# Optimization experiments

Hardware: AMD Instinct MI355X
Metric: run time of the kernel (lower is better)

## Reference

```python
import jax, jax.numpy as jnp
import numpy as np


def _gcn_conv(x, edge_index, W, b):
    # PyG GCNConv: h = x @ W; out = D^{-1/2}(A+I)D^{-1/2} h + b
    N = x.shape[0]
    src, dst = edge_index[0], edge_index[1]
    # degree with self-loops (edge weights = 1)
    deg = jax.ops.segment_sum(jnp.ones(src.shape[0], x.dtype), dst, num_segments=N) + 1.0
    dis = jax.lax.rsqrt(deg)  # deg >= 1 so finite
    h = x @ W  # [N, F_out]
    norm = dis[src] * dis[dst]  # [E]
    msg = h[src] * norm[:, None]  # [E, F_out] -- dominant memory traffic
    agg = jax.ops.segment_sum(msg, dst, num_segments=N)
    # self-loop contribution: norm_ii = dis_i^2
    out = agg + h * (dis * dis)[:, None] + b
    return out


def setup_inputs() -> dict:
    key = jax.random.key(0)
    k1, k2, k3, k4, k5, k6 = jax.random.split(key, 6)
    N, E = 100000, 1600000
    in_ch, hid, out_ch = 256, 128, 64  # hid = 2*out_channels
    x = jax.random.normal(k1, (N, in_ch), dtype=jnp.float32)
    edge_index = jax.random.randint(k2, (2, E), 0, N, dtype=jnp.int64)
    # Glorot-style init for GCN weights, zero bias (PyG default)
    W1 = jax.random.normal(k3, (in_ch, hid), dtype=jnp.float32) / np.sqrt(in_ch)
    b1 = jnp.zeros((hid,), jnp.float32)
    W2 = jax.random.normal(k4, (hid, out_ch), dtype=jnp.float32) / np.sqrt(hid)
    b2 = jnp.zeros((out_ch,), jnp.float32)
    return {"x": x, "edge_index": edge_index, "W1": W1, "b1": b1, "W2": W2, "b2": b2}


def reference(x, edge_index, W1, b1, W2, b2):
    # Encoder.forward: k=2 layers of activation(GCNConv(x, edge_index))
    h = jax.nn.relu(_gcn_conv(x, edge_index, W1, b1))
    h = jax.nn.relu(_gcn_conv(h, edge_index, W2, b2))
    return h
```

## Files before the change

kernel.cpp:

```cpp
#include <hip/hip_runtime.h>
#include <math.h>

#define THREADS 256
#define HIST_ILP 8
#define EPB_SHIFT 11

static inline int cdiv(long long a, long long b) { return (int)((a + b - 1) / b); }

typedef __attribute__((ext_vector_type(8))) short bf16x8;
typedef __attribute__((ext_vector_type(4))) float f32x4;

__device__ inline unsigned f2bf_rne_u(float f) {
    unsigned u = __builtin_bit_cast(unsigned, f);
    return (u + 0x7FFFu + ((u >> 16) & 1u)) >> 16;
}
__device__ inline float bfu2f(unsigned h) {
    unsigned u = h << 16;
    return __builtin_bit_cast(float, u);
}


__device__ __forceinline__ void bfrag_unit(const float* __restrict__ W, short* __restrict__ frag,
                                           int NCT, int ctks, int lane) {
    int Nn = NCT * 16;
    int ct = ctks % NCT;
    int ks = ctks / NCT;
    int colc = ct * 16 + (lane & 15);
    int kbase = ks * 32 + (lane >> 4) * 8;
    short* base = frag + (size_t)ctks * 1024 + lane * 8;
    #pragma unroll
    for (int j = 0; j < 8; ++j) {
        float v = W[(size_t)(kbase + j) * Nn + colc];
        unsigned h = f2bf_rne_u(v);
        base[j] = (short)h;
        base[512 + j] = (short)f2bf_rne_u(v - bfu2f(h));
    }
}

__device__ __forceinline__ void hist_body8(const int* __restrict__ dst, int* __restrict__ deg,
                                           int* __restrict__ rank, int E, int hb) {
    int base = (hb << EPB_SHIFT) + (int)threadIdx.x * HIST_ILP;
    if (base + HIST_ILP - 1 < E) {
        int4 d0 = *(const int4*)(dst + base);
        int4 d1 = *(const int4*)(dst + base + 4);
        int4 r0, r1;
        r0.x = atomicAdd(&deg[d0.x], 1);
        r0.y = atomicAdd(&deg[d0.y], 1);
        r0.z = atomicAdd(&deg[d0.z], 1);
        r0.w = atomicAdd(&deg[d0.w], 1);
        r1.x = atomicAdd(&deg[d1.x], 1);
        r1.y = atomicAdd(&deg[d1.y], 1);
        r1.z = atomicAdd(&deg[d1.z], 1);
        r1.w = atomicAdd(&deg[d1.w], 1);
        *(int4*)(rank + base) = r0;
        *(int4*)(rank + base + 4) = r1;
    } else {
        for (int e = base; e < E; ++e) rank[e] = atomicAdd(&deg[dst[e]], 1);
    }
}

template<int NCT, int KS>
__device__ __forceinline__ void gemm_body(const float* __restrict__ A, const short* __restrict__ Bfrag,
                                          unsigned short* __restrict__ H, int M, int blk) {
    constexpr int K = KS * 32;
    constexpr int Nn = NCT * 16;
    const int lane = threadIdx.x & 63;
    const int wave = threadIdx.x >> 6;
    const int rowBase = blk * 128 + wave * 32;
    const int arow0 = rowBase + (lane & 15);
    const int kgrp = (lane >> 4) * 8;

    f32x4 acc[2][NCT] = {};

    for (int ks = 0; ks < KS; ++ks) {
        const int kbase = ks * 32 + kgrp;
        bf16x8 ahi[2], alo[2];
        #pragma unroll
        for (int t = 0; t < 2; ++t) {
            int r = arow0 + t * 16;
            if (r >= M) r = M - 1;
            const float* ap = A + (size_t)r * K + kbase;
            float4 v0 = *(const float4*)ap;
            float4 v1 = *(const float4*)(ap + 4);
            float av[8] = {v0.x, v0.y, v0.z, v0.w, v1.x, v1.y, v1.z, v1.w};
            #pragma unroll
            for (int j = 0; j < 8; ++j) {
                unsigned h = f2bf_rne_u(av[j]);
                ahi[t][j] = (short)h;
                alo[t][j] = (short)f2bf_rne_u(av[j] - bfu2f(h));
            }
        }
        #pragma unroll
        for (int ct = 0; ct < NCT; ++ct) {
            const short* bp = Bfrag + (size_t)(ks * NCT + ct) * 1024 + lane * 8;
            bf16x8 bhi = *(const bf16x8*)bp;
            bf16x8 blo = *(const bf16x8*)(bp + 512);
            #pragma unroll
            for (int t = 0; t < 2; ++t) {
                acc[t][ct] = __builtin_amdgcn_mfma_f32_16x16x32_bf16(ahi[t], bhi, acc[t][ct], 0, 0, 0);
                acc[t][ct] = __builtin_amdgcn_mfma_f32_16x16x32_bf16(ahi[t], blo, acc[t][ct], 0, 0, 0);
                acc[t][ct] = __builtin_amdgcn_mfma_f32_16x16x32_bf16(alo[t], bhi, acc[t][ct], 0, 0, 0);
            }
        }
    }

    const int drow0 = rowBase + (lane >> 4) * 4;
    #pragma unroll
    for (int t = 0; t < 2; ++t) {
        #pragma unroll
        for (int r = 0; r < 4; ++r) {
            int row = drow0 + t * 16 + r;
            if (row < M) {
                unsigned short* hp = H + (size_t)row * Nn + (lane & 15);
                #pragma unroll
                for (int ct = 0; ct < NCT; ++ct)
                    hp[ct * 16] = (unsigned short)f2bf_rne_u(acc[t][ct][r]);
            }
        }
    }
}

template<int NCT, int KS>
__device__ __forceinline__ void gemm_bf16A_body(const unsigned short* __restrict__ A,
                                                const short* __restrict__ Bfrag,
                                                unsigned short* __restrict__ H, int M, int blk) {
    constexpr int K = KS * 32;
    constexpr int Nn = NCT * 16;
    const int lane = threadIdx.x & 63;
    const int wave = threadIdx.x >> 6;
    const int rowBase = blk * 128 + wave * 32;
    const int arow0 = rowBase + (lane & 15);
    const int kgrp = (lane >> 4) * 8;

    f32x4 acc[2][NCT] = {};

    for (int ks = 0; ks < KS; ++ks) {
        const int kbase = ks * 32 + kgrp;
        bf16x8 a[2];
        #pragma unroll
        for (int t = 0; t < 2; ++t) {
            int r = arow0 + t * 16;
            if (r >= M) r = M - 1;
            a[t] = *(const bf16x8*)(A + (size_t)r * K + kbase);
        }
        #pragma unroll
        for (int ct = 0; ct < NCT; ++ct) {
            const short* bp = Bfrag + (size_t)(ks * NCT + ct) * 1024 + lane * 8;
            bf16x8 bhi = *(const bf16x8*)bp;
            bf16x8 blo = *(const bf16x8*)(bp + 512);
            #pragma unroll
            for (int t = 0; t < 2; ++t) {
                acc[t][ct] = __builtin_amdgcn_mfma_f32_16x16x32_bf16(a[t], bhi, acc[t][ct], 0, 0, 0);
                acc[t][ct] = __builtin_amdgcn_mfma_f32_16x16x32_bf16(a[t], blo, acc[t][ct], 0, 0, 0);
            }
        }
    }

    const int drow0 = rowBase + (lane >> 4) * 4;
    #pragma unroll
    for (int t = 0; t < 2; ++t) {
        #pragma unroll
        for (int r = 0; r < 4; ++r) {
            int row = drow0 + t * 16 + r;
            if (row < M) {
                unsigned short* hp = H + (size_t)row * Nn + (lane & 15);
                #pragma unroll
                for (int ct = 0; ct < NCT; ++ct)
                    hp[ct * 16] = (unsigned short)f2bf_rne_u(acc[t][ct][r]);
            }
        }
    }
}


__global__ __launch_bounds__(THREADS)
void zero_bfrag_kernel(int* __restrict__ deg, int N,
                       const float* __restrict__ W1, short* __restrict__ bf1,
                       const float* __restrict__ W2, short* __restrict__ bf2, int nbZero) {
    int b = (int)blockIdx.x;
    if (b < nbZero) {
        int base = (b * THREADS + (int)threadIdx.x) * 4;
        if (base + 3 < N) {
            *(int4*)(deg + base) = make_int4(0, 0, 0, 0);
        } else {
            for (int i = base; i < N; ++i) deg[i] = 0;
        }
    } else {
        int u = (b - nbZero) * 4 + ((int)threadIdx.x >> 6);
        int lane = threadIdx.x & 63;
        if (u < 64) bfrag_unit(W1, bf1, 8, u, lane);
        else if (u < 80) bfrag_unit(W2, bf2, 4, u - 64, lane);
    }
}

__global__ __launch_bounds__(THREADS)
void hist_gemm1_kernel(const int* __restrict__ dst, int* __restrict__ deg,
                       int* __restrict__ rank, int E,
                       const float* __restrict__ A, const short* __restrict__ Bfrag,
                       unsigned short* __restrict__ H, int M,
                       int nbHist, int nbGemm) {
    int b = (int)blockIdx.x;
    int total = nbHist + nbGemm;
    long long t = (long long)b * nbGemm;
    int gBefore = (int)(t / total);
    bool isG = (((long long)(b + 1) * nbGemm) / total) > gBefore;
    if (isG) gemm_body<8, 8>(A, Bfrag, H, M, gBefore);
    else     hist_body8(dst, deg, rank, E, b - gBefore);
}

__global__ __launch_bounds__(THREADS)
void fill_col_rank_kernel(const int* __restrict__ src, const int* __restrict__ dst,
                          const int* __restrict__ rank, const int* __restrict__ rowptr,
                          int* __restrict__ col, int E) {
    int base = ((int)blockIdx.x * THREADS + (int)threadIdx.x) * 4;
    if (base + 3 < E) {
        int4 d = *(const int4*)(dst + base);
        int4 r = *(const int4*)(rank + base);
        int4 s = *(const int4*)(src + base);
        col[rowptr[d.x] + r.x] = s.x;
        col[rowptr[d.y] + r.y] = s.y;
        col[rowptr[d.z] + r.z] = s.z;
        col[rowptr[d.w] + r.w] = s.w;
    } else {
        for (int e = base; e < E; ++e)
            col[rowptr[dst[e]] + rank[e]] = src[e];
    }
}

__global__ __launch_bounds__(THREADS)
void mfma_gemm2_kernel(const unsigned short* __restrict__ A, const short* __restrict__ Bfrag,
                       unsigned short* __restrict__ H, int M) {
    gemm_bf16A_body<4, 4>(A, Bfrag, H, M, (int)blockIdx.x);
}


#define SCAN_BLOCK 256
#define SCAN_ITEMS 4

__global__ __launch_bounds__(SCAN_BLOCK)
void scan_block_kernel(const int* __restrict__ in, int* __restrict__ out,
                       int* __restrict__ blockSums, float* __restrict__ dis, int n) {
    __shared__ int sdata[SCAN_BLOCK];
    int base = blockIdx.x * (SCAN_BLOCK * SCAN_ITEMS);
    int tid = threadIdx.x;
    int v[SCAN_ITEMS];
    int sum = 0;
    #pragma unroll
    for (int k = 0; k < SCAN_ITEMS; ++k) {
        int idx = base + tid * SCAN_ITEMS + k;
        v[k] = (idx < n) ? in[idx] : 0;
        if (idx < n) dis[idx] = rsqrtf((float)v[k] + 1.0f);
        sum += v[k];
    }
    sdata[tid] = sum;
    __syncthreads();
    for (int off = 1; off < SCAN_BLOCK; off <<= 1) {
        int t = (tid >= off) ? sdata[tid - off] : 0;
        __syncthreads();
        sdata[tid] += t;
        __syncthreads();
    }
    if (tid == SCAN_BLOCK - 1) blockSums[blockIdx.x] = sdata[SCAN_BLOCK - 1];
    int run = (tid == 0) ? 0 : sdata[tid - 1];
    #pragma unroll
    for (int k = 0; k < SCAN_ITEMS; ++k) {
        int idx = base + tid * SCAN_ITEMS + k;
        if (idx < n) out[idx] = run;
        run += v[k];
    }
}

__global__ __launch_bounds__(SCAN_BLOCK)
void scan_sums_kernel(int* __restrict__ blockSums, int nB) {
    __shared__ int sdata[SCAN_BLOCK];
    int tid = threadIdx.x;
    sdata[tid] = (tid < nB) ? blockSums[tid] : 0;
    __syncthreads();
    for (int off = 1; off < SCAN_BLOCK; off <<= 1) {
        int t = (tid >= off) ? sdata[tid - off] : 0;
        __syncthreads();
        sdata[tid] += t;
        __syncthreads();
    }
    int excl = (tid == 0) ? 0 : sdata[tid - 1];
    if (tid < nB) blockSums[tid] = excl;
}

__global__ __launch_bounds__(SCAN_BLOCK)
void scan_add_kernel(int* __restrict__ out, const int* __restrict__ blockSums,
                     int n, int E) {
    int base = blockIdx.x * (SCAN_BLOCK * SCAN_ITEMS);
    int add = blockSums[blockIdx.x];
    #pragma unroll
    for (int k = 0; k < SCAN_ITEMS; ++k) {
        int idx = base + threadIdx.x * SCAN_ITEMS + k;
        if (idx < n) out[idx] += add;
    }
    if (blockIdx.x == 0 && threadIdx.x == 0) out[n] = E;
}


template<int F, int VEC, bool OUTBF16>
__global__ __launch_bounds__(THREADS)
void gather_bf16_kernel(const unsigned short* __restrict__ g, const int* __restrict__ col,
                        const int* __restrict__ rowptr, const float* __restrict__ dis,
                        const float* __restrict__ bias, void* __restrict__ outv, int N) {
    int wid = (int)((blockIdx.x * (long long)blockDim.x + threadIdx.x) >> 6);
    wid = __builtin_amdgcn_readfirstlane(wid);
    const int lane = threadIdx.x & 63;
    if (wid >= N) return;
    const float di = dis[wid];
    const int loff = lane * VEC;

    float acc0 = 0.0f, acc1 = 0.0f;

    auto loadrow = [&](int s) -> unsigned {
        const unsigned short* p = g + (size_t)s * F + loff;
        if (VEC == 2) return *(const unsigned*)p;
        else return (unsigned)*p;
    };
    auto addconv = [&](unsigned u, float w) {
        if (VEC == 2) {
            acc0 += w * bfu2f(u & 0xFFFFu);
            acc1 += w * __builtin_bit_cast(float, u & 0xFFFF0000u);
        } else {
            acc0 += w * bfu2f(u);
        }
    };

    addconv(loadrow(wid), di);

    int start = __builtin_amdgcn_readfirstlane(rowptr[wid]);
    int end   = __builtin_amdgcn_readfirstlane(rowptr[wid + 1]);
    const int* c = col + start;
    int rem = end - start;

    if (rem >= 8) {
        int s0 = __builtin_amdgcn_readfirstlane(c[0]);
        int s1 = __builtin_amdgcn_readfirstlane(c[1]);
        int s2 = __builtin_amdgcn_readfirstlane(c[2]);
        int s3 = __builtin_amdgcn_readfirstlane(c[3]);
        int s4 = __builtin_amdgcn_readfirstlane(c[4]);
        int s5 = __builtin_amdgcn_readfirstlane(c[5]);
        int s6 = __builtin_amdgcn_readfirstlane(c[6]);
        int s7 = __builtin_amdgcn_readfirstlane(c[7]);
        float w0 = dis[s0], w1 = dis[s1], w2 = dis[s2], w3 = dis[s3];
        float w4 = dis[s4], w5 = dis[s5], w6 = dis[s6], w7 = dis[s7];
        unsigned u0 = loadrow(s0), u1 = loadrow(s1), u2 = loadrow(s2), u3 = loadrow(s3);
        unsigned u4 = loadrow(s4), u5 = loadrow(s5), u6 = loadrow(s6), u7 = loadrow(s7);
        c += 8; rem -= 8;
        while (rem >= 8) {
            int t0 = __builtin_amdgcn_readfirstlane(c[0]);
            int t1 = __builtin_amdgcn_readfirstlane(c[1]);
            int t2 = __builtin_amdgcn_readfirstlane(c[2]);
            int t3 = __builtin_amdgcn_readfirstlane(c[3]);
            int t4 = __builtin_amdgcn_readfirstlane(c[4]);
            int t5 = __builtin_amdgcn_readfirstlane(c[5]);
            int t6 = __builtin_amdgcn_readfirstlane(c[6]);
            int t7 = __builtin_amdgcn_readfirstlane(c[7]);
            float x0 = dis[t0], x1 = dis[t1], x2 = dis[t2], x3 = dis[t3];
            float x4 = dis[t4], x5 = dis[t5], x6 = dis[t6], x7 = dis[t7];
            unsigned v0 = loadrow(t0), v1 = loadrow(t1), v2 = loadrow(t2), v3 = loadrow(t3);
            unsigned v4 = loadrow(t4), v5 = loadrow(t5), v6 = loadrow(t6), v7 = loadrow(t7);
            addconv(u0, w0); addconv(u1, w1); addconv(u2, w2); addconv(u3, w3);
            addconv(u4, w4); addconv(u5, w5); addconv(u6, w6); addconv(u7, w7);
            u0 = v0; u1 = v1; u2 = v2; u3 = v3;
            u4 = v4; u5 = v5; u6 = v6; u7 = v7;
            w0 = x0; w1 = x1; w2 = x2; w3 = x3;
            w4 = x4; w5 = x5; w6 = x6; w7 = x7;
            c += 8; rem -= 8;
        }
        addconv(u0, w0); addconv(u1, w1); addconv(u2, w2); addconv(u3, w3);
        addconv(u4, w4); addconv(u5, w5); addconv(u6, w6); addconv(u7, w7);
    }
    if (rem >= 4) {
        int s0 = __builtin_amdgcn_readfirstlane(c[0]);
        int s1 = __builtin_amdgcn_readfirstlane(c[1]);
        int s2 = __builtin_amdgcn_readfirstlane(c[2]);
        int s3 = __builtin_amdgcn_readfirstlane(c[3]);
        float w0 = dis[s0], w1 = dis[s1], w2 = dis[s2], w3 = dis[s3];
        unsigned u0 = loadrow(s0), u1 = loadrow(s1), u2 = loadrow(s2), u3 = loadrow(s3);
        addconv(u0, w0); addconv(u1, w1); addconv(u2, w2); addconv(u3, w3);
        c += 4; rem -= 4;
    }
    while (rem > 0) {
        int s = __builtin_amdgcn_readfirstlane(c[0]);
        addconv(loadrow(s), dis[s]);
        ++c; --rem;
    }

    float v0 = fmaxf(di * acc0 + bias[loff], 0.0f);
    if (OUTBF16) {
        unsigned short* orow = (unsigned short*)outv + (size_t)wid * F + loff;
        if (VEC == 2) {
            float v1 = fmaxf(di * acc1 + bias[loff + 1], 0.0f);
            unsigned pack = f2bf_rne_u(v0) | (f2bf_rne_u(v1) << 16);
            *(unsigned*)orow = pack;
        } else {
            *orow = (unsigned short)f2bf_rne_u(v0);
        }
    } else {
        float* orow = (float*)outv + (size_t)wid * F + loff;
        if (VEC == 2) {
            float v1 = fmaxf(di * acc1 + bias[loff + 1], 0.0f);
            *(float2*)orow = make_float2(v0, v1);
        } else {
            *orow = v0;
        }
    }
}


#define BM 64
#define BN 64
#define BK 16

__global__ __launch_bounds__(THREADS)
void sgemm_kernel(const float* __restrict__ A, const float* __restrict__ B,
                  float* __restrict__ C, int M, int N, int K) {
    __shared__ float As[BK][BM + 1];
    __shared__ float Bs[BK][BN + 1];

    const int tid = threadIdx.x;
    const int tr = tid / 16;
    const int tc = tid % 16;
    const int rowBase = blockIdx.y * BM;
    const int colBase = blockIdx.x * BN;

    float acc[4][4] = {};

    for (int k0 = 0; k0 < K; k0 += BK) {
        #pragma unroll
        for (int i = tid; i < BM * BK; i += THREADS) {
            int r = i / BK, c = i % BK;
            int gr = rowBase + r;
            As[c][r] = (gr < M) ? A[(size_t)gr * K + k0 + c] : 0.0f;
        }
        #pragma unroll
        for (int i = tid; i < BK * BN; i += THREADS) {
            int r = i / BN, c = i % BN;
            Bs[r][c] = B[(size_t)(k0 + r) * N + colBase + c];
        }
        __syncthreads();

        #pragma unroll
        for (int k = 0; k < BK; ++k) {
            float a[4], b[4];
            #pragma unroll
            for (int m = 0; m < 4; ++m) a[m] = As[k][tr * 4 + m];
            #pragma unroll
            for (int n = 0; n < 4; ++n) b[n] = Bs[k][tc * 4 + n];
            #pragma unroll
            for (int m = 0; m < 4; ++m)
                #pragma unroll
                for (int n = 0; n < 4; ++n)
                    acc[m][n] += a[m] * b[n];
        }
        __syncthreads();
    }

    #pragma unroll
    for (int m = 0; m < 4; ++m) {
        int gr = rowBase + tr * 4 + m;
        if (gr >= M) continue;
        #pragma unroll
        for (int n = 0; n < 4; ++n) {
            C[(size_t)gr * N + colBase + tc * 4 + n] = acc[m][n];
        }
    }
}

__global__ __launch_bounds__(THREADS)
void init_agg_kernel(const float* __restrict__ h, const float* __restrict__ dis,
                     float* __restrict__ agg, int N, int F) {
    int i = blockIdx.x * blockDim.x + threadIdx.x;
    int total = N * (F / 4);
    if (i >= total) return;
    int node = i / (F / 4);
    float d = dis[node];
    float w = d * d;
    float4 v = ((const float4*)h)[i];
    v.x *= w; v.y *= w; v.z *= w; v.w *= w;
    ((float4*)agg)[i] = v;
}

__global__ __launch_bounds__(THREADS)
void edge_scatter_kernel(const float* __restrict__ h, const int* __restrict__ src,
                         const int* __restrict__ dst, const float* __restrict__ dis,
                         float* __restrict__ agg, int E, int F) {
    int lanesPerEdge = F / 4;
    int tid = blockIdx.x * blockDim.x + threadIdx.x;
    int e = tid / lanesPerEdge;
    int c = tid % lanesPerEdge;
    if (e >= E) return;
    int s = src[e];
    int d = dst[e];
    float w = dis[s] * dis[d];
    float4 hv = ((const float4*)(h + (size_t)s * F))[c];
    float* ap = agg + (size_t)d * F + (size_t)c * 4;
    atomicAdd(ap + 0, hv.x * w);
    atomicAdd(ap + 1, hv.y * w);
    atomicAdd(ap + 2, hv.z * w);
    atomicAdd(ap + 3, hv.w * w);
}

__global__ __launch_bounds__(THREADS)
void finalize_kernel(const float* __restrict__ agg, const float* __restrict__ b,
                     float* __restrict__ out, int N, int F) {
    int i = blockIdx.x * blockDim.x + threadIdx.x;
    int total = N * (F / 4);
    if (i >= total) return;
    int c4 = i % (F / 4);
    float4 bv = ((const float4*)b)[c4];
    float4 v = ((const float4*)agg)[i];
    v.x = fmaxf(v.x + bv.x, 0.0f);
    v.y = fmaxf(v.y + bv.y, 0.0f);
    v.z = fmaxf(v.z + bv.z, 0.0f);
    v.w = fmaxf(v.w + bv.w, 0.0f);
    ((float4*)out)[i] = v;
}

__global__ __launch_bounds__(THREADS)
void fdeg_kernel(const int* __restrict__ dst, float* __restrict__ deg, int E) {
    int i = blockIdx.x * blockDim.x + threadIdx.x;
    if (i < E) atomicAdd(&deg[dst[i]], 1.0f);
}

__global__ __launch_bounds__(THREADS)
void fdis_kernel(float* __restrict__ deg, int N) {
    int i = blockIdx.x * blockDim.x + threadIdx.x;
    if (i < N) deg[i] = rsqrtf(deg[i] + 1.0f);
}


extern "C" void kernel_launch(void* const* d_in, const int* in_sizes, int n_in,
                              void* d_out, int out_size, void* d_ws, size_t ws_size,
                              hipStream_t stream) {
    const float* x  = (const float*)d_in[0];
    const int*   ei = (const int*)d_in[1];
    const float* W1 = (const float*)d_in[2];
    const float* b1 = (const float*)d_in[3];
    const float* W2 = (const float*)d_in[4];
    const float* b2 = (const float*)d_in[5];

    const int E    = in_sizes[1] / 2;
    const int hid  = in_sizes[3];
    const int outc = in_sizes[5];
    const int inc  = in_sizes[2] / hid;
    const int N    = in_sizes[0] / inc;

    const int* src = ei;
    const int* dst = ei + E;
    float* out = (float*)d_out;
    char* ws = (char*)d_ws;

    auto al = [](size_t v) { return (v + 255) & ~(size_t)255; };
    size_t o_dis  = 0;
    size_t o_deg  = al(o_dis + (size_t)N * 4);
    size_t o_rp   = al(o_deg + (size_t)N * 4);
    size_t o_bs   = al(o_rp + ((size_t)N + 1) * 4);
    size_t o_col  = al(o_bs + 4096);
    size_t o_rank = al(o_col + (size_t)E * 4);
    size_t o_bf1  = al(o_rank + (size_t)E * 4);
    size_t o_bf2  = al(o_bf1 + 131072);
    size_t o_G    = al(o_bf2 + 32768);
    size_t o_B    = al(o_G + (size_t)N * hid * 2);
    size_t need   = o_B + (size_t)N * hid * 2;

    if (ws_size >= need && N <= SCAN_BLOCK * SCAN_BLOCK * SCAN_ITEMS &&
        hid == 128 && outc == 64 && inc == 256) {
        float* dis    = (float*)(ws + o_dis);
        int*   deg    = (int*)(ws + o_deg);
        int*   rowptr = (int*)(ws + o_rp);
        int*   bsums  = (int*)(ws + o_bs);
        int*   col    = (int*)(ws + o_col);
        int*   rank   = (int*)(ws + o_rank);
        short* bf1    = (short*)(ws + o_bf1);
        short* bf2    = (short*)(ws + o_bf2);
        unsigned short* gbuf = (unsigned short*)(ws + o_G);
        unsigned short* out1 = (unsigned short*)(ws + o_B);

        const int nbZero  = cdiv(N, 4 * THREADS);
        const int nbHist  = cdiv(E, THREADS * HIST_ILP);
        const int nbGemm1 = cdiv(N, 128);
        const int nbFill  = cdiv(E, 4 * THREADS);

        zero_bfrag_kernel<<<nbZero + 20, THREADS, 0, stream>>>(deg, N, W1, bf1, W2, bf2, nbZero);

        hist_gemm1_kernel<<<nbHist + nbGemm1, THREADS, 0, stream>>>(
            dst, deg, rank, E, x, bf1, gbuf, N, nbHist, nbGemm1);

        int nB = cdiv(N, SCAN_BLOCK * SCAN_ITEMS);
        scan_block_kernel<<<nB, SCAN_BLOCK, 0, stream>>>(deg, rowptr, bsums, dis, N);
        scan_sums_kernel<<<1, SCAN_BLOCK, 0, stream>>>(bsums, nB);
        scan_add_kernel<<<nB, SCAN_BLOCK, 0, stream>>>(rowptr, bsums, N, E);

        fill_col_rank_kernel<<<nbFill, THREADS, 0, stream>>>(src, dst, rank, rowptr, col, E);

        gather_bf16_kernel<128, 2, true><<<cdiv((long long)N * 64, THREADS), THREADS, 0, stream>>>(
            gbuf, col, rowptr, dis, b1, out1, N);

        mfma_gemm2_kernel<<<cdiv(N, 128), THREADS, 0, stream>>>(out1, bf2, gbuf, N);
        gather_bf16_kernel<64, 1, false><<<cdiv((long long)N * 64, THREADS), THREADS, 0, stream>>>(
            gbuf, col, rowptr, dis, b2, out, N);
        return;
    }

    float* dis = (float*)ws;
    size_t off1 = ((size_t)N * 4 + 255) & ~(size_t)255;
    float* h1 = (float*)(ws + off1);
    size_t off2 = off1 + ((((size_t)N * hid * 4) + 255) & ~(size_t)255);
    float* agg1 = (float*)(ws + off2);
    float* h2   = agg1;
    float* agg2 = agg1 + (size_t)N * outc;

    hipMemsetAsync(dis, 0, (size_t)N * 4, stream);
    fdeg_kernel<<<cdiv(E, THREADS), THREADS, 0, stream>>>(dst, dis, E);
    fdis_kernel<<<cdiv(N, THREADS), THREADS, 0, stream>>>(dis, N);

    {
        dim3 grid(hid / BN, cdiv(N, BM));
        sgemm_kernel<<<grid, THREADS, 0, stream>>>(x, W1, h1, N, hid, inc);
    }
    init_agg_kernel<<<cdiv((long long)N * hid / 4, THREADS), THREADS, 0, stream>>>(h1, dis, agg1, N, hid);
    edge_scatter_kernel<<<cdiv((long long)E * (hid / 4), THREADS), THREADS, 0, stream>>>(
        h1, src, dst, dis, agg1, E, hid);
    finalize_kernel<<<cdiv((long long)N * hid / 4, THREADS), THREADS, 0, stream>>>(agg1, b1, h1, N, hid);

    {
        dim3 grid(outc / BN, cdiv(N, BM));
        sgemm_kernel<<<grid, THREADS, 0, stream>>>(h1, W2, h2, N, outc, hid);
    }
    init_agg_kernel<<<cdiv((long long)N * outc / 4, THREADS), THREADS, 0, stream>>>(h2, dis, agg2, N, outc);
    edge_scatter_kernel<<<cdiv((long long)E * (outc / 4), THREADS), THREADS, 0, stream>>>(
        h2, src, dst, dis, agg2, E, outc);
    finalize_kernel<<<cdiv((long long)N * outc / 4, THREADS), THREADS, 0, stream>>>(agg2, b2, out, N, outc);
}
```

Measured before the change: 245.0 us.

## Build CSR via bucketed scatter with shared-memory per-bucket histogram and fill

```diff
diff --git a/kernel.cpp b/kernel.cpp
--- a/kernel.cpp
+++ b/kernel.cpp
@@ -4,6 +4,8 @@
 #define THREADS 256
 #define HIST_ILP 8
 #define EPB_SHIFT 11
+#define BSHIFT 8
+#define BCAP 6144
 
 static inline int cdiv(long long a, long long b) { return (int)((a + b - 1) / b); }
 
@@ -37,25 +39,31 @@
     }
 }
 
-__device__ __forceinline__ void hist_body8(const int* __restrict__ dst, int* __restrict__ deg,
-                                           int* __restrict__ rank, int E, int hb) {
+__device__ __forceinline__ void bscat_body(const int* __restrict__ src, const int* __restrict__ dst,
+                                           int* __restrict__ cursor, int2* __restrict__ pairs,
+                                           int E, int hb) {
     int base = (hb << EPB_SHIFT) + (int)threadIdx.x * HIST_ILP;
     if (base + HIST_ILP - 1 < E) {
         int4 d0 = *(const int4*)(dst + base);
         int4 d1 = *(const int4*)(dst + base + 4);
-        int4 r0, r1;
-        r0.x = atomicAdd(&deg[d0.x], 1);
-        r0.y = atomicAdd(&deg[d0.y], 1);
-        r0.z = atomicAdd(&deg[d0.z], 1);
-        r0.w = atomicAdd(&deg[d0.w], 1);
-        r1.x = atomicAdd(&deg[d1.x], 1);
-        r1.y = atomicAdd(&deg[d1.y], 1);
-        r1.z = atomicAdd(&deg[d1.z], 1);
-        r1.w = atomicAdd(&deg[d1.w], 1);
-        *(int4*)(rank + base) = r0;
-        *(int4*)(rank + base + 4) = r1;
+        int4 s0 = *(const int4*)(src + base);
+        int4 s1 = *(const int4*)(src + base + 4);
+        int b, p;
+        b = d0.x >> BSHIFT; p = atomicAdd(&cursor[b], 1); if (p < BCAP) pairs[(size_t)b * BCAP + p] = make_int2(s0.x, d0.x);
+        b = d0.y >> BSHIFT; p = atomicAdd(&cursor[b], 1); if (p < BCAP) pairs[(size_t)b * BCAP + p] = make_int2(s0.y, d0.y);
+        b = d0.z >> BSHIFT; p = atomicAdd(&cursor[b], 1); if (p < BCAP) pairs[(size_t)b * BCAP + p] = make_int2(s0.z, d0.z);
+        b = d0.w >> BSHIFT; p = atomicAdd(&cursor[b], 1); if (p < BCAP) pairs[(size_t)b * BCAP + p] = make_int2(s0.w, d0.w);
+        b = d1.x >> BSHIFT; p = atomicAdd(&cursor[b], 1); if (p < BCAP) pairs[(size_t)b * BCAP + p] = make_int2(s1.x, d1.x);
+        b = d1.y >> BSHIFT; p = atomicAdd(&cursor[b], 1); if (p < BCAP) pairs[(size_t)b * BCAP + p] = make_int2(s1.y, d1.y);
+        b = d1.z >> BSHIFT; p = atomicAdd(&cursor[b], 1); if (p < BCAP) pairs[(size_t)b * BCAP + p] = make_int2(s1.z, d1.z);
+        b = d1.w >> BSHIFT; p = atomicAdd(&cursor[b], 1); if (p < BCAP) pairs[(size_t)b * BCAP + p] = make_int2(s1.w, d1.w);
     } else {
-        for (int e = base; e < E; ++e) rank[e] = atomicAdd(&deg[dst[e]], 1);
+        for (int e = base; e < E; ++e) {
+            int d = dst[e];
+            int b = d >> BSHIFT;
+            int p = atomicAdd(&cursor[b], 1);
+            if (p < BCAP) pairs[(size_t)b * BCAP + p] = make_int2(src[e], d);
+        }
     }
 }
 
@@ -174,19 +182,14 @@
 
 
 __global__ __launch_bounds__(THREADS)
-void zero_bfrag_kernel(int* __restrict__ deg, int N,
+void zero_bfrag_kernel(int* __restrict__ cursor, int nbkt,
                        const float* __restrict__ W1, short* __restrict__ bf1,
-                       const float* __restrict__ W2, short* __restrict__ bf2, int nbZero) {
+                       const float* __restrict__ W2, short* __restrict__ bf2) {
     int b = (int)blockIdx.x;
-    if (b < nbZero) {
-        int base = (b * THREADS + (int)threadIdx.x) * 4;
-        if (base + 3 < N) {
-            *(int4*)(deg + base) = make_int4(0, 0, 0, 0);
-        } else {
-            for (int i = base; i < N; ++i) deg[i] = 0;
-        }
+    if (b == 0) {
+        for (int i = threadIdx.x; i < nbkt; i += THREADS) cursor[i] = 0;
     } else {
-        int u = (b - nbZero) * 4 + ((int)threadIdx.x >> 6);
+        int u = (b - 1) * 4 + ((int)threadIdx.x >> 6);
         int lane = threadIdx.x & 63;
         if (u < 64) bfrag_unit(W1, bf1, 8, u, lane);
         else if (u < 80) bfrag_unit(W2, bf2, 4, u - 64, lane);
@@ -194,36 +197,50 @@
 }
 
 __global__ __launch_bounds__(THREADS)
-void hist_gemm1_kernel(const int* __restrict__ dst, int* __restrict__ deg,
-                       int* __restrict__ rank, int E,
-                       const float* __restrict__ A, const short* __restrict__ Bfrag,
-                       unsigned short* __restrict__ H, int M,
-                       int nbHist, int nbGemm) {
+void bscat_gemm1_kernel(const int* __restrict__ src, const int* __restrict__ dst,
+                        int* __restrict__ cursor, int2* __restrict__ pairs, int E,
+                        const float* __restrict__ A, const short* __restrict__ Bfrag,
+                        unsigned short* __restrict__ H, int M,
+                        int nbScat, int nbGemm) {
     int b = (int)blockIdx.x;
-    int total = nbHist + nbGemm;
+    int total = nbScat + nbGemm;
     long long t = (long long)b * nbGemm;
     int gBefore = (int)(t / total);
     bool isG = (((long long)(b + 1) * nbGemm) / total) > gBefore;
     if (isG) gemm_body<8, 8>(A, Bfrag, H, M, gBefore);
-    else     hist_body8(dst, deg, rank, E, b - gBefore);
-}
-
-__global__ __launch_bounds__(THREADS)
-void fill_col_rank_kernel(const int* __restrict__ src, const int* __restrict__ dst,
-                          const int* __restrict__ rank, const int* __restrict__ rowptr,
-                          int* __restrict__ col, int E) {
-    int base = ((int)blockIdx.x * THREADS + (int)threadIdx.x) * 4;
-    if (base + 3 < E) {
-        int4 d = *(const int4*)(dst + base);
-        int4 r = *(const int4*)(rank + base);
-        int4 s = *(const int4*)(src + base);
-        col[rowptr[d.x] + r.x] = s.x;
-        col[rowptr[d.y] + r.y] = s.y;
-        col[rowptr[d.z] + r.z] = s.z;
-        col[rowptr[d.w] + r.w] = s.w;
-    } else {
-        for (int e = base; e < E; ++e)
-            col[rowptr[dst[e]] + rank[e]] = src[e];
+    else     bscat_body(src, dst, cursor, pairs, E, b - gBefore);
+}
+
+__global__ __launch_bounds__(THREADS)
+void bucket_hist_kernel(const int* __restrict__ cursor, const int2* __restrict__ pairs,
+                        int* __restrict__ rankArr, int* __restrict__ deg, int N) {
+    int bkt = (int)blockIdx.x;
+    __shared__ int ldeg[256];
+    ldeg[threadIdx.x] = 0;
+    __syncthreads();
+    int cnt = cursor[bkt]; if (cnt > BCAP) cnt = BCAP;
+    for (int i = (int)threadIdx.x; i < cnt; i += THREADS) {
+        int2 p = pairs[(size_t)bkt * BCAP + i];
+        rankArr[(size_t)bkt * BCAP + i] = atomicAdd(&ldeg[p.y & 255], 1);
+    }
+    __syncthreads();
+    int node = (bkt << BSHIFT) + (int)threadIdx.x;
+    if (node < N) deg[node] = ldeg[threadIdx.x];
+}
+
+__global__ __launch_bounds__(THREADS)
+void bucket_fill_kernel(const int* __restrict__ cursor, const int2* __restrict__ pairs,
+                        const int* __restrict__ rankArr, const int* __restrict__ rowptr,
+                        int* __restrict__ col, int N) {
+    int bkt = (int)blockIdx.x;
+    __shared__ int rp[256];
+    int node = (bkt << BSHIFT) + (int)threadIdx.x;
+    rp[threadIdx.x] = (node < N) ? rowptr[node] : 0;
+    __syncthreads();
+    int cnt = cursor[bkt]; if (cnt > BCAP) cnt = BCAP;
+    for (int i = (int)threadIdx.x; i < cnt; i += THREADS) {
+        int2 p = pairs[(size_t)bkt * BCAP + i];
+        col[rp[p.y & 255] + rankArr[(size_t)bkt * BCAP + i]] = p.x;
     }
 }
 
@@ -554,48 +571,55 @@
     float* out = (float*)d_out;
     char* ws = (char*)d_ws;
 
+    const int NBKT = (N + 255) >> BSHIFT;
+
     auto al = [](size_t v) { return (v + 255) & ~(size_t)255; };
-    size_t o_dis  = 0;
-    size_t o_deg  = al(o_dis + (size_t)N * 4);
-    size_t o_rp   = al(o_deg + (size_t)N * 4);
-    size_t o_bs   = al(o_rp + ((size_t)N + 1) * 4);
-    size_t o_col  = al(o_bs + 4096);
-    size_t o_rank = al(o_col + (size_t)E * 4);
-    size_t o_bf1  = al(o_rank + (size_t)E * 4);
-    size_t o_bf2  = al(o_bf1 + 131072);
-    size_t o_G    = al(o_bf2 + 32768);
-    size_t o_B    = al(o_G + (size_t)N * hid * 2);
-    size_t need   = o_B + (size_t)N * hid * 2;
+    size_t o_dis   = 0;
+    size_t o_deg   = al(o_dis + (size_t)N * 4);
+    size_t o_rp    = al(o_deg + (size_t)N * 4);
+    size_t o_bs    = al(o_rp + ((size_t)N + 1) * 4);
+    size_t o_cur   = al(o_bs + 4096);
+    size_t o_col   = al(o_cur + (size_t)NBKT * 4);
+    size_t o_pairs = al(o_col + (size_t)E * 4);
+    size_t o_rank  = al(o_pairs + (size_t)NBKT * BCAP * 8);
+    size_t o_bf1   = al(o_rank + (size_t)NBKT * BCAP * 4);
+    size_t o_bf2   = al(o_bf1 + 131072);
+    size_t o_G     = al(o_bf2 + 32768);
+    size_t o_B     = al(o_G + (size_t)N * hid * 2);
+    size_t need    = o_B + (size_t)N * hid * 2;
 
     if (ws_size >= need && N <= SCAN_BLOCK * SCAN_BLOCK * SCAN_ITEMS &&
-        hid == 128 && outc == 64 && inc == 256) {
+        hid == 128 && outc == 64 && inc == 256 &&
+        (long long)E <= (long long)NBKT * 4200) {
         float* dis    = (float*)(ws + o_dis);
         int*   deg    = (int*)(ws + o_deg);
         int*   rowptr = (int*)(ws + o_rp);
         int*   bsums  = (int*)(ws + o_bs);
+        int*   cursor = (int*)(ws + o_cur);
         int*   col    = (int*)(ws + o_col);
-        int*   rank   = (int*)(ws + o_rank);
+        int2*  pairs  = (int2*)(ws + o_pairs);
+        int*   rankA  = (int*)(ws + o_rank);
         short* bf1    = (short*)(ws + o_bf1);
         short* bf2    = (short*)(ws + o_bf2);
         unsigned short* gbuf = (unsigned short*)(ws + o_G);
         unsigned short* out1 = (unsigned short*)(ws + o_B);
 
-        const int nbZero  = cdiv(N, 4 * THREADS);
-        const int nbHist  = cdiv(E, THREADS * HIST_ILP);
+        const int nbScat  = cdiv(E, THREADS * HIST_ILP);
         const int nbGemm1 = cdiv(N, 128);
-        const int nbFill  = cdiv(E, 4 * THREADS);
-
-        zero_bfrag_kernel<<<nbZero + 20, THREADS, 0, stream>>>(deg, N, W1, bf1, W2, bf2, nbZero);
-
-        hist_gemm1_kernel<<<nbHist + nbGemm1, THREADS, 0, stream>>>(
-            dst, deg, rank, E, x, bf1, gbuf, N, nbHist, nbGemm1);
+
+        zero_bfrag_kernel<<<1 + 20, THREADS, 0, stream>>>(cursor, NBKT, W1, bf1, W2, bf2);
+
+        bscat_gemm1_kernel<<<nbScat + nbGemm1, THREADS, 0, stream>>>(
+            src, dst, cursor, pairs, E, x, bf1, gbuf, N, nbScat, nbGemm1);
+
+        bucket_hist_kernel<<<NBKT, THREADS, 0, stream>>>(cursor, pairs, rankA, deg, N);
 
         int nB = cdiv(N, SCAN_BLOCK * SCAN_ITEMS);
         scan_block_kernel<<<nB, SCAN_BLOCK, 0, stream>>>(deg, rowptr, bsums, dis, N);
         scan_sums_kernel<<<1, SCAN_BLOCK, 0, stream>>>(bsums, nB);
         scan_add_kernel<<<nB, SCAN_BLOCK, 0, stream>>>(rowptr, bsums, N, E);
 
-        fill_col_rank_kernel<<<nbFill, THREADS, 0, stream>>>(src, dst, rank, rowptr, col, E);
+        bucket_fill_kernel<<<NBKT, THREADS, 0, stream>>>(cursor, pairs, rankA, rowptr, col, N);
 
         gather_bf16_kernel<128, 2, true><<<cdiv((long long)N * 64, THREADS), THREADS, 0, stream>>>(
             gbuf, col, rowptr, dis, b1, out1, N);
```

After: 726.0 us. 196% more time.
